# Optimization experiments

Measured on AMD Instinct MI355X. Metric: run time of the kernel, lower is better.

The kernel has to match this reference:

```python
import jax, jax.numpy as jnp
import numpy as np

NUM_HEADS = 16

def setup_inputs() -> dict:
    key = jax.random.key(0)
    ks = jax.random.split(key, 6)
    d_in, d_out = 1024, 1024
    x = jax.random.normal(ks[0], (4, 2048, d_in), dtype=jnp.float32)
    s = 0.02
    Wq = jax.random.normal(ks[1], (d_in, d_out), dtype=jnp.float32) * s
    Wk = jax.random.normal(ks[2], (d_in, d_out), dtype=jnp.float32) * s
    Wv = jax.random.normal(ks[3], (d_in, d_out), dtype=jnp.float32) * s
    Wo = jax.random.normal(ks[4], (d_out, d_out), dtype=jnp.float32) * s
    bo = jnp.zeros((d_out,), dtype=jnp.float32)
    return {"x": x, "Wq": Wq, "Wk": Wk, "Wv": Wv, "Wo": Wo, "bo": bo}

def reference(x, Wq, Wk, Wv, Wo, bo):
    b, n, _ = x.shape
    h = NUM_HEADS
    hd = Wq.shape[1] // h
    # project and split heads: [b, h, n, hd]
    def split(t):
        return t.reshape(b, n, h, hd).transpose(0, 2, 1, 3)
    q = split(x @ Wq)
    k = split(x @ Wk)
    v = split(x @ Wv)
    scores = jnp.einsum('bhqd,bhkd->bhqk', q, k)
    causal = jnp.tril(jnp.ones((n, n), dtype=bool))  # True = keep
    scores = jnp.where(causal, scores, -jnp.inf)
    att = jax.nn.softmax(scores / jnp.sqrt(jnp.float32(hd)), axis=-1)
    out = jnp.einsum('bhqk,bhkd->bhqd', att, v)
    out = out.transpose(0, 2, 1, 3).reshape(b, n, h * hd)
    return out @ Wo + bo
```

## Files before the change

### kernel.cpp

```cpp
#include <hip/hip_runtime.h>
#include <math.h>

namespace {
constexpr int NB = 4;
constexpr int NS = 2048;
constexpr int DM = 1024;
constexpr int NH = 16;
constexpr int DH = 64;
constexpr int M  = NB * NS;

typedef __bf16 bf16x8 __attribute__((ext_vector_type(8)));
typedef float  floatx4 __attribute__((ext_vector_type(4)));

__device__ __forceinline__ ushort f2bf(float f) {
    uint u = __float_as_uint(f);
    return (ushort)((u + 0x7FFFu + ((u >> 16) & 1u)) >> 16);
}
__device__ __forceinline__ uint cvt_pk_bf16(float lo, float hi) {
    uint r;
    asm("v_cvt_pk_bf16_f32 %0, %1, %2" : "=v"(r) : "v"(lo), "v"(hi));
    return r;
}
__device__ __forceinline__ float fast_exp2(float x) {
#if __has_builtin(__builtin_amdgcn_exp2f)
    return __builtin_amdgcn_exp2f(x);
#else
    return exp2f(x);
#endif
}
__device__ __forceinline__ void gload16(const void* g, void* l) {
    __builtin_amdgcn_global_load_lds(
        (const __attribute__((address_space(1))) unsigned int*)g,
        (__attribute__((address_space(3))) unsigned int*)l, 16, 0, 0);
}

__global__ __launch_bounds__(256) void conv_x_k(const float* __restrict__ in,
                                                ushort* __restrict__ out) {
    int i = blockIdx.x * 256 + threadIdx.x;
    float4 v = ((const float4*)in)[i];
    ushort4 o;
    o.x = f2bf(v.x); o.y = f2bf(v.y); o.z = f2bf(v.z); o.w = f2bf(v.w);
    ((ushort4*)out)[i] = o;
}

__global__ __launch_bounds__(256) void conv_wt4_k(const float* __restrict__ W0,
                                                  const float* __restrict__ W1,
                                                  const float* __restrict__ W2,
                                                  const float* __restrict__ W3,
                                                  ushort* __restrict__ T0,
                                                  ushort* __restrict__ T1,
                                                  ushort* __restrict__ T2,
                                                  ushort* __restrict__ T3) {
    __shared__ float tile[64][65];
    const int z = blockIdx.z;
    const float* W = (z == 0) ? W0 : (z == 1) ? W1 : (z == 2) ? W2 : W3;
    ushort* Wt     = (z == 0) ? T0 : (z == 1) ? T1 : (z == 2) ? T2 : T3;
    const int t = threadIdx.x;
    const int k0 = blockIdx.y * 64, n0 = blockIdx.x * 64;
    #pragma unroll
    for (int i = 0; i < 16; ++i) {
        int idx = i * 256 + t, r = idx >> 6, c = idx & 63;
        tile[r][c] = W[(size_t)(k0 + r) * DM + n0 + c];
    }
    __syncthreads();
    #pragma unroll
    for (int i = 0; i < 16; ++i) {
        int idx = i * 256 + t, r = idx >> 6, c = idx & 63;
        Wt[(size_t)(n0 + r) * DM + k0 + c] = f2bf(tile[c][r]);
    }
}

template<int MODE>
__global__ __launch_bounds__(256) void mm_bf16_k(const ushort* __restrict__ A,
                                                 const ushort* __restrict__ Bt,
                                                 const float* __restrict__ bias,
                                                 void* __restrict__ outp,
                                                 float oscale) {
    __shared__ __align__(16) ushort As[2 * 128 * 32];
    __shared__ __align__(16) ushort Bs[2 * 128 * 32];
    const int t  = threadIdx.x;
    const int l  = t & 63;
    const int w  = t >> 6;
    const int wr = w >> 1, wc = w & 1;
    const int lr = l & 15, lg = l >> 4;
    const int row0 = blockIdx.y * 128;
    const int col0 = blockIdx.x * 128;

    floatx4 acc[4][4];
    #pragma unroll
    for (int m = 0; m < 4; ++m)
        #pragma unroll
        for (int n = 0; n < 4; ++n) acc[m][n] = (floatx4){0.f, 0.f, 0.f, 0.f};

    #pragma unroll
    for (int i = 0; i < 2; ++i) {
        int c = i * 256 + t, r = c >> 2, cb = (c & 3) * 16;
        gload16((const char*)A  + (size_t)(row0 + r) * 2048 + cb,
                (char*)As + c * 16);
        gload16((const char*)Bt + (size_t)(col0 + r) * 2048 + cb,
                (char*)Bs + c * 16);
    }
    int cur = 0;

    for (int k0 = 0; k0 < DM; k0 += 32) {
        __syncthreads();
        if (k0 + 32 < DM) {
            const int nb = cur ^ 1;
            #pragma unroll
            for (int i = 0; i < 2; ++i) {
                int c = i * 256 + t, r = c >> 2, cb = (c & 3) * 16;
                gload16((const char*)A  + (size_t)(row0 + r) * 2048 + (size_t)(k0 + 32) * 2 + cb,
                        (char*)As + nb * 8192 + c * 16);
                gload16((const char*)Bt + (size_t)(col0 + r) * 2048 + (size_t)(k0 + 32) * 2 + cb,
                        (char*)Bs + nb * 8192 + c * 16);
            }
        }

        const ushort* abase = As + cur * 4096 + (wr * 64 + lr) * 32 + lg * 8;
        const ushort* bbase = Bs + cur * 4096 + (wc * 64 + lr) * 32 + lg * 8;
        bf16x8 af[4], bfv[4];
        #pragma unroll
        for (int m = 0; m < 4; ++m)
            af[m] = *(const bf16x8*)(abase + m * 16 * 32);
        #pragma unroll
        for (int n = 0; n < 4; ++n)
            bfv[n] = *(const bf16x8*)(bbase + n * 16 * 32);
        #pragma unroll
        for (int m = 0; m < 4; ++m)
            #pragma unroll
            for (int n = 0; n < 4; ++n)
                acc[m][n] = __builtin_amdgcn_mfma_f32_16x16x32_bf16(
                    af[m], bfv[n], acc[m][n], 0, 0, 0);
        cur ^= 1;
    }

    #pragma unroll
    for (int m = 0; m < 4; ++m) {
        #pragma unroll
        for (int n = 0; n < 4; ++n) {
            floatx4 d = acc[m][n];
            #pragma unroll
            for (int r = 0; r < 4; ++r) {
                int grow = row0 + wr * 64 + m * 16 + lg * 4 + r;
                int gcol = col0 + wc * 64 + n * 16 + lr;
                if (MODE == 1) {
                    ((float*)outp)[(size_t)grow * DM + gcol] = d[r] + bias[gcol];
                } else if (MODE == 2) {
                    int h = grow >> 6,  dd = grow & 63;
                    int b = gcol >> 11, nn = gcol & (NS - 1);
                    int k6 = nn & 63;
                    int np = (nn & ~63) | (k6 & 3) | (((k6 >> 5) & 1) << 2) |
                             (((k6 >> 2) & 3) << 3) | (((k6 >> 4) & 1) << 5);
                    ((ushort*)outp)[((size_t)(b * NH + h) * DH + dd) * NS + np] = f2bf(d[r]);
                } else {
                    int which = gcol >> 10;
                    int col = gcol & 1023;
                    int b = grow >> 11, nn = grow & (NS - 1);
                    int h = col >> 6,  dd = col & 63;
                    float sc = which ? 1.f : oscale;
                    ((ushort*)outp)[(size_t)which * M * DM +
                        (((size_t)(b * NH + h)) * NS + nn) * DH + dd] = f2bf(d[r] * sc);
                }
            }
        }
    }
}

__global__ __launch_bounds__(256, 4) void attn_k(const ushort* __restrict__ Q,
                                                 const ushort* __restrict__ K,
                                                 const ushort* __restrict__ Vt,
                                                 ushort* __restrict__ O) {
    __shared__ __align__(16) ushort K_lds[2 * 64 * 64];
    __shared__ __align__(16) ushort V_lds[2 * 64 * 64];

    const int t    = threadIdx.x;
    const int w    = t >> 6;
    const int l    = t & 63;
    const int lr   = l & 15;
    const int lg   = l >> 4;
    const int bh   = blockIdx.x;
    const int qblk = 15 - blockIdx.y;
    const size_t base = (size_t)bh * NS * DH;
    const int b = bh >> 4, h = bh & 15;

    const int srow_lo = l >> 3;
    const int gs      = (l & 7) ^ srow_lo;

    const int qbase  = qblk * 128;
    const int qmin_w = qbase + w * 32;
    const int qmax_w = qmin_w + 31;
    const int ntiles = 2 * (qblk + 1);

    bf16x8 qb[2][2];
    #pragma unroll
    for (int nq = 0; nq < 2; ++nq)
        #pragma unroll
        for (int kk2 = 0; kk2 < 2; ++kk2)
            qb[nq][kk2] = *(const bf16x8*)&Q[base +
                (size_t)(qbase + w * 32 + nq * 16 + lr) * DH + kk2 * 32 + lg * 8];

    uint4 ones_u = make_uint4(0x3F803F80u, 0x3F803F80u, 0x3F803F80u, 0x3F803F80u);
    bf16x8 ones_b = *(const bf16x8*)&ones_u;

    floatx4 acc[2][4];
    #pragma unroll
    for (int nq = 0; nq < 2; ++nq)
        #pragma unroll
        for (int nd = 0; nd < 4; ++nd) acc[nq][nd] = (floatx4){0.f, 0.f, 0.f, 0.f};
    floatx4 accl[2];
    accl[0] = (floatx4){0.f, 0.f, 0.f, 0.f};
    accl[1] = (floatx4){0.f, 0.f, 0.f, 0.f};
    const floatx4 z4 = (floatx4){0.f, 0.f, 0.f, 0.f};

    #pragma unroll
    for (int i = 0; i < 2; ++i) {
        int cc = w + i * 4, rr = cc * 8 + srow_lo;
        gload16((const char*)(K + base + (size_t)rr * DH) + gs * 16,
                (char*)K_lds + cc * 1024 + l * 16);
        gload16((const char*)(Vt + base + (size_t)rr * NS) + gs * 16,
                (char*)V_lds + cc * 1024 + l * 16);
    }
    int cur = 0;

    for (int tile = 0; tile < ntiles; ++tile) {
        const int kv0 = tile * 64;
        __syncthreads();
        if (tile + 1 < ntiles) {
            const int kvn = kv0 + 64;
            const int nb = cur ^ 1;
            #pragma unroll
            for (int i = 0; i < 2; ++i) {
                int cc = w + i * 4, rr = cc * 8 + srow_lo;
                gload16((const char*)(K + base + (size_t)(kvn + rr) * DH) + gs * 16,
                        (char*)K_lds + nb * 8192 + cc * 1024 + l * 16);
                gload16((const char*)(Vt + base + (size_t)rr * NS + kvn) + gs * 16,
                        (char*)V_lds + nb * 8192 + cc * 1024 + l * 16);
            }
        }

        if (kv0 <= qmax_w) {
            floatx4 s[4][2];
            __builtin_amdgcn_s_setprio(1);
            {
                bf16x8 ka[4];
                #pragma unroll
                for (int m = 0; m < 4; ++m)
                    ka[m] = *(const bf16x8*)((const char*)K_lds + cur * 8192 +
                        (m * 16 + lr) * 128 + ((lg ^ (lr & 7)) * 16));
                #pragma unroll
                for (int m = 0; m < 4; ++m)
                    #pragma unroll
                    for (int nq = 0; nq < 2; ++nq)
                        s[m][nq] = __builtin_amdgcn_mfma_f32_16x16x32_bf16(
                            ka[m], qb[nq][0], z4, 0, 0, 0);
                #pragma unroll
                for (int m = 0; m < 4; ++m)
                    ka[m] = *(const bf16x8*)((const char*)K_lds + cur * 8192 +
                        (m * 16 + lr) * 128 + (((4 + lg) ^ (lr & 7)) * 16));
                #pragma unroll
                for (int m = 0; m < 4; ++m)
                    #pragma unroll
                    for (int nq = 0; nq < 2; ++nq)
                        s[m][nq] = __builtin_amdgcn_mfma_f32_16x16x32_bf16(
                            ka[m], qb[nq][1], s[m][nq], 0, 0, 0);
            }
            __builtin_amdgcn_s_setprio(0);

            const bool need_mask = (kv0 + 63 > qmin_w);
            const int kb0 = kv0 + lg * 4;
            #pragma unroll
            for (int nq = 0; nq < 2; ++nq) {
                const int qn = qmin_w + nq * 16 + lr;
                #pragma unroll
                for (int m = 0; m < 4; ++m) {
                    #pragma unroll
                    for (int r = 0; r < 4; ++r) {
                        float v = s[m][nq][r];
                        if (need_mask)
                            v = ((kb0 + m * 16 + r) > qn) ? -INFINITY : v;
                        s[m][nq][r] = fast_exp2(v);
                    }
                }
            }

            __builtin_amdgcn_s_setprio(1);
            #pragma unroll
            for (int kk2 = 0; kk2 < 2; ++kk2) {
                const int m0 = kk2, m1 = kk2 + 2;
                bf16x8 vb[4];
                #pragma unroll
                for (int nd = 0; nd < 4; ++nd)
                    vb[nd] = *(const bf16x8*)((const char*)V_lds + cur * 8192 +
                        (nd * 16 + lr) * 128 + (((kk2 * 4 + lg) ^ (lr & 7)) * 16));
                #pragma unroll
                for (int nq = 0; nq < 2; ++nq) {
                    uint4 pk;
                    pk.x = cvt_pk_bf16(s[m0][nq][0], s[m0][nq][1]);
                    pk.y = cvt_pk_bf16(s[m0][nq][2], s[m0][nq][3]);
                    pk.z = cvt_pk_bf16(s[m1][nq][0], s[m1][nq][1]);
                    pk.w = cvt_pk_bf16(s[m1][nq][2], s[m1][nq][3]);
                    bf16x8 pa = *(const bf16x8*)&pk;
                    #pragma unroll
                    for (int nd = 0; nd < 4; ++nd)
                        acc[nq][nd] = __builtin_amdgcn_mfma_f32_16x16x32_bf16(
                            pa, vb[nd], acc[nq][nd], 0, 0, 0);
                    accl[nq] = __builtin_amdgcn_mfma_f32_16x16x32_bf16(
                        pa, ones_b, accl[nq], 0, 0, 0);
                }
            }
            __builtin_amdgcn_s_setprio(0);
        }
        cur ^= 1;
    }

    #pragma unroll
    for (int nq = 0; nq < 2; ++nq) {
        #pragma unroll
        for (int r = 0; r < 4; ++r) {
            float inv = 1.f / accl[nq][r];
            int q = qbase + w * 32 + nq * 16 + lg * 4 + r;
            ushort* op = &O[((size_t)(b * NS + q)) * DM + h * DH + lr];
            op[0]  = f2bf(acc[nq][0][r] * inv);
            op[16] = f2bf(acc[nq][1][r] * inv);
            op[32] = f2bf(acc[nq][2][r] * inv);
            op[48] = f2bf(acc[nq][3][r] * inv);
        }
    }
}

}

extern "C" void kernel_launch(void* const* d_in, const int* in_sizes, int n_in,
                              void* d_out, int out_size, void* d_ws, size_t ws_size,
                              hipStream_t stream) {
    const float* x  = (const float*)d_in[0];
    const float* Wq = (const float*)d_in[1];
    const float* Wk = (const float*)d_in[2];
    const float* Wv = (const float*)d_in[3];
    const float* Wo = (const float*)d_in[4];
    const float* bo = (const float*)d_in[5];
    float* out = (float*)d_out;

    ushort* xb  = (ushort*)d_ws;
    ushort* WqT = xb  + (size_t)M * DM;
    ushort* WkT = WqT + (size_t)DM * DM;
    ushort* WvT = WkT + (size_t)DM * DM;
    ushort* WoT = WvT + (size_t)DM * DM;
    ushort* Qb  = WoT + (size_t)DM * DM;
    ushort* Kb  = Qb  + (size_t)M * DM;
    ushort* Vtg = Kb  + (size_t)M * DM;
    ushort* Ab  = Vtg + (size_t)M * DM;

    const float SCALE_Q = 0.125f * 1.4426950408889634f;

    conv_x_k<<<M * DM / 4 / 256, 256, 0, stream>>>(x, xb);
    conv_wt4_k<<<dim3(DM / 64, DM / 64, 4), 256, 0, stream>>>(
        Wq, Wk, Wv, Wo, WqT, WkT, WvT, WoT);

    mm_bf16_k<3><<<dim3(2048 / 128, M / 128), 256, 0, stream>>>(xb, WqT, nullptr, Qb, SCALE_Q);
    mm_bf16_k<2><<<dim3(M / 128, DM / 128), 256, 0, stream>>>(WvT, xb, nullptr, Vtg, 1.f);
    attn_k<<<dim3(NB * NH, 16), 256, 0, stream>>>(Qb, Kb, Vtg, Ab);
    mm_bf16_k<1><<<dim3(DM / 128, M / 128), 256, 0, stream>>>(Ab, WoT, bo, out, 1.f);
}
```

Before: 169.4 us.

## Swizzle GEMM tile order, rebalance attention q-block order, precompute KV load pointers

The GEMM kernel remaps linear block IDs with an XCD-style stride-8 swizzle, so consecutive workgroups on the same chiplet share A and B tiles in L2. The attention kernel reorders causal q-blocks across blockIdx.y so heavy and light blocks interleave, aiming for better load balance across CUs. KV tile loads now use precomputed, incrementing pointers instead of recomputing addresses every iteration, which cuts integer address arithmetic. The swizzle assumes the workgroup count is divisible by 8.

Result: faster. 163.1 us (median of 3 runs) (-3.7%).

```diff
diff --git a/kernel.cpp b/kernel.cpp
--- a/kernel.cpp
+++ b/kernel.cpp
@@ -83,8 +83,12 @@
     const int w  = t >> 6;
     const int wr = w >> 1, wc = w & 1;
     const int lr = l & 15, lg = l >> 4;
-    const int row0 = blockIdx.y * 128;
-    const int col0 = blockIdx.x * 128;
+
+    const int nwg = gridDim.x * gridDim.y;
+    const int lin = blockIdx.y * gridDim.x + blockIdx.x;
+    const int id2 = (lin & 7) * (nwg >> 3) + (lin >> 3);
+    const int row0 = (id2 / gridDim.x) * 128;
+    const int col0 = (id2 % gridDim.x) * 128;
 
     floatx4 acc[4][4];
     #pragma unroll
@@ -179,7 +183,11 @@
     const int lr   = l & 15;
     const int lg   = l >> 4;
     const int bh   = blockIdx.x;
-    const int qblk = 15 - blockIdx.y;
+    const int yp = blockIdx.y & 3, yr = blockIdx.y >> 2;
+    const int qblk = (yr == 0) ? 15 - yp
+                   : (yr == 1) ? 8 + yp
+                   : (yr == 2) ? 4 + (yp ^ 1)
+                               : (yp ^ 2);
     const size_t base = (size_t)bh * NS * DH;
     const int b = bh >> 4, h = bh & 15;
 
@@ -212,30 +220,28 @@
     accl[1] = (floatx4){0.f, 0.f, 0.f, 0.f};
     const floatx4 z4 = (floatx4){0.f, 0.f, 0.f, 0.f};
 
-    #pragma unroll
-    for (int i = 0; i < 2; ++i) {
-        int cc = w + i * 4, rr = cc * 8 + srow_lo;
-        gload16((const char*)(K + base + (size_t)rr * DH) + gs * 16,
-                (char*)K_lds + cc * 1024 + l * 16);
-        gload16((const char*)(Vt + base + (size_t)rr * NS) + gs * 16,
-                (char*)V_lds + cc * 1024 + l * 16);
-    }
+    const char* kg0 = (const char*)(K + base + (size_t)(w * 8 + srow_lo) * DH) + gs * 16;
+    const char* kg1 = kg0 + (size_t)32 * DH * 2;
+    const char* vg0 = (const char*)(Vt + base + (size_t)(w * 8 + srow_lo) * NS) + gs * 16;
+    const char* vg1 = vg0 + (size_t)32 * NS * 2;
+    char* kl0 = (char*)K_lds + w * 1024 + l * 16;
+    char* kl1 = kl0 + 4096;
+    char* vl0 = (char*)V_lds + w * 1024 + l * 16;
+    char* vl1 = vl0 + 4096;
+
+    gload16(kg0, kl0); gload16(vg0, vl0);
+    gload16(kg1, kl1); gload16(vg1, vl1);
+    kg0 += 8192; kg1 += 8192; vg0 += 128; vg1 += 128;
     int cur = 0;
 
     for (int tile = 0; tile < ntiles; ++tile) {
         const int kv0 = tile * 64;
         __syncthreads();
         if (tile + 1 < ntiles) {
-            const int kvn = kv0 + 64;
             const int nb = cur ^ 1;
-            #pragma unroll
-            for (int i = 0; i < 2; ++i) {
-                int cc = w + i * 4, rr = cc * 8 + srow_lo;
-                gload16((const char*)(K + base + (size_t)(kvn + rr) * DH) + gs * 16,
-                        (char*)K_lds + nb * 8192 + cc * 1024 + l * 16);
-                gload16((const char*)(Vt + base + (size_t)rr * NS + kvn) + gs * 16,
-                        (char*)V_lds + nb * 8192 + cc * 1024 + l * 16);
-            }
+            gload16(kg0, kl0 + nb * 8192); gload16(vg0, vl0 + nb * 8192);
+            gload16(kg1, kl1 + nb * 8192); gload16(vg1, vl1 + nb * 8192);
+            kg0 += 8192; kg1 += 8192; vg0 += 128; vg1 += 128;
         }
 
         if (kv0 <= qmax_w) {
```
